# Kernel tuning notes

Measured on AMD Instinct MI355X. Metric: run time of the kernel, lower is better.

## Reference

```python
import jax, jax.numpy as jnp
import numpy as np

B, S, D, H = 8, 2048, 1024, 64

def setup_inputs() -> dict:
    key = jax.random.key(0)
    k1, k2, k3, k4 = jax.random.split(key, 4)
    idx = jax.random.normal(k1, (B, S, D), dtype=jnp.float32)
    # nn.Linear(D, H, bias=False) weights, stored as [D, H] for x @ W
    Wk = jax.random.normal(k2, (D, H), dtype=jnp.float32) * (1.0 / np.sqrt(D))
    Wq = jax.random.normal(k3, (D, H), dtype=jnp.float32) * (1.0 / np.sqrt(D))
    Wv = jax.random.normal(k4, (D, H), dtype=jnp.float32) * (1.0 / np.sqrt(D))
    return {"idx": idx, "Wk": Wk, "Wq": Wq, "Wv": Wv}

def reference(idx, Wk, Wq, Wv):
    b, s, d = idx.shape
    k = idx @ Wk  # [b, s, h]
    q = idx @ Wq
    v = idx @ Wv
    # NOTE: original scales by embedding_dim**-0.5, not head_size**-0.5
    wei = jnp.einsum('bqh,bkh->bqk', q, k) * (d ** -0.5)
    causal = jnp.tril(jnp.ones((s, s), dtype=bool))
    wei = jnp.where(causal, wei, -jnp.inf)
    attn = jax.nn.softmax(wei, axis=-1)  # dropout p=0.0 -> identity
    return jnp.einsum('bqk,bkh->bqh', attn, v)
```

## Files before the change

kernel.cpp:

```cpp
#include <hip/hip_runtime.h>

typedef __attribute__((ext_vector_type(8))) short short8;
typedef __attribute__((ext_vector_type(4))) short short4v;
typedef __attribute__((ext_vector_type(4))) float f32x4;

#define MFMA_16x16x32_BF16(A, B, C) __builtin_amdgcn_mfma_f32_16x16x32_bf16(A, B, C, 0, 0, 0)

__device__ __forceinline__ unsigned short f2bf(float x) {
    unsigned int u = __builtin_bit_cast(unsigned int, x);
    u = (u + 0x7FFFu + ((u >> 16) & 1u)) >> 16;
    return (unsigned short)u;
}

__global__ __launch_bounds__(256) void wconv_kernel(const float* __restrict__ Wk,
                                                    const float* __restrict__ Wq,
                                                    const float* __restrict__ Wv,
                                                    unsigned short* __restrict__ Wt) {
    const int n = blockIdx.x;
    const float* W = (n < 64) ? Wk : (n < 128) ? Wq : Wv;
    const int col = n & 63;
    const int sw = (n & 7) << 3;
    for (int k = threadIdx.x; k < 1024; k += 256) {
        const int kd = (k & ~56) | ((k ^ sw) & 56);
        Wt[(size_t)n * 1024 + kd] = f2bf(W[(size_t)k * 64 + col]);
    }
}

__global__ __launch_bounds__(256) void proj_kernel(const float* __restrict__ X,
                                                   const unsigned short* __restrict__ Wt,
                                                   unsigned short* __restrict__ Kb,
                                                   unsigned short* __restrict__ Qb,
                                                   unsigned short* __restrict__ Vtg) {
    __shared__ __attribute__((aligned(16))) unsigned short Al[32 * 72];
    __shared__ __attribute__((aligned(16))) unsigned short Wl[192 * 64];
    const int t = threadIdx.x;
    const int w = t >> 6, lane = t & 63, lr = lane & 15, g = lane >> 4;
    const int wr = w >> 1, wc = w & 1;
    const int r0 = blockIdx.x * 32;

    f32x4 acc[6] = {};

    const int ar = t >> 3, aj = t & 7;
    const float* xsrc = X + (size_t)(r0 + ar) * 1024 + aj * 8;

    float4 a0 = *(const float4*)xsrc;
    float4 a1 = *(const float4*)(xsrc + 4);
    uint4 aw;
    aw.x = (unsigned)f2bf(a0.x) | ((unsigned)f2bf(a0.y) << 16);
    aw.y = (unsigned)f2bf(a0.z) | ((unsigned)f2bf(a0.w) << 16);
    aw.z = (unsigned)f2bf(a1.x) | ((unsigned)f2bf(a1.y) << 16);
    aw.w = (unsigned)f2bf(a1.z) | ((unsigned)f2bf(a1.w) << 16);

    for (int k0 = 0; k0 < 1024; k0 += 64) {
        __syncthreads();
#pragma unroll
        for (int i = 0; i < 6; ++i) {
            const int q = t + 256 * i;
            const unsigned short* src = Wt + (size_t)(q >> 3) * 1024 + k0 + (q & 7) * 8;
            __builtin_amdgcn_global_load_lds((const __attribute__((address_space(1))) void*)src,
                                             (__attribute__((address_space(3))) void*)&Wl[q * 8],
                                             16, 0, 0);
        }
        *(uint4*)&Al[ar * 72 + aj * 8] = aw;
        __syncthreads();

        const bool more = (k0 + 64) < 1024;
        if (more) {
            a0 = *(const float4*)(xsrc + k0 + 64);
            a1 = *(const float4*)(xsrc + k0 + 68);
        }

        short8 af[2];
        af[0] = *(const short8*)&Al[(16 * wr + lr) * 72 + 8 * g];
        af[1] = *(const short8*)&Al[(16 * wr + lr) * 72 + 32 + 8 * g];
#pragma unroll
        for (int c = 0; c < 6; ++c) {
            const int row = 96 * wc + 16 * c + lr;
#pragma unroll
            for (int sub = 0; sub < 2; ++sub) {
                const int cs = (4 * sub + g) ^ (lr & 7);
                short8 wf = *(const short8*)&Wl[row * 64 + cs * 8];
                acc[c] = MFMA_16x16x32_BF16(af[sub], wf, acc[c]);
            }
        }

        if (more) {
            aw.x = (unsigned)f2bf(a0.x) | ((unsigned)f2bf(a0.y) << 16);
            aw.y = (unsigned)f2bf(a0.z) | ((unsigned)f2bf(a0.w) << 16);
            aw.z = (unsigned)f2bf(a1.x) | ((unsigned)f2bf(a1.y) << 16);
            aw.w = (unsigned)f2bf(a1.z) | ((unsigned)f2bf(a1.w) << 16);
        }
    }

    const int bb = r0 >> 11;
    const int sb0 = (r0 & 2047) + 16 * wr;
    const int row = r0 + 16 * wr + 4 * g;
#pragma unroll
    for (int c = 0; c < 6; ++c) {
        const int n = 96 * wc + 16 * c;
        if (n < 64) {
#pragma unroll
            for (int r = 0; r < 4; ++r)
                Kb[(size_t)(row + r) * 64 + n + lr] = f2bf(acc[c][r]);
        } else if (n < 128) {
#pragma unroll
            for (int r = 0; r < 4; ++r)
                Qb[(size_t)(row + r) * 64 + (n - 64) + lr] = f2bf(acc[c][r]);
        } else {
            const int h = n - 128 + lr;
            uint2 e;
            e.x = (unsigned)f2bf(acc[c][0]) | ((unsigned)f2bf(acc[c][1]) << 16);
            e.y = (unsigned)f2bf(acc[c][2]) | ((unsigned)f2bf(acc[c][3]) << 16);
            *(uint2*)(Vtg + (size_t)bb * 64 * 2048 + (size_t)h * 2048 + sb0 + 4 * g) = e;
        }
    }
}

__global__ __launch_bounds__(512, 2) void attn_kernel(const unsigned short* __restrict__ Kb,
                                                      const unsigned short* __restrict__ Qb,
                                                      const unsigned short* __restrict__ Vtg,
                                                      float* __restrict__ out) {
    __shared__ __attribute__((aligned(16))) float Pacc[16][32][68];
    __shared__ float Pml[2][16][32];

    const int t = threadIdx.x;
    const int w = t >> 6, lane = t & 63;
    const int lr = lane & 15, g = lane >> 4;
    const int p = blockIdx.x, b = blockIdx.y;
    const int nhi = 64 - p;
    const int q0h = (63 - p) * 32, q0l = p * 32;
    const size_t rowbase = (size_t)b * 2048;
    const size_t vbase = (size_t)b * 64 * 2048;
    const float NEG_INF = -__builtin_inff();
    const float SCALE2 = 0.03125f * 1.4426950408889634f;

    short8 qfH[2][2], qfL[2][2];
#pragma unroll
    for (int sub = 0; sub < 2; ++sub)
#pragma unroll
        for (int hh = 0; hh < 2; ++hh) {
            qfH[sub][hh] = *(const short8*)(Qb + (rowbase + q0h + 16 * sub + lr) * 64 + 32 * hh + 8 * g);
            qfL[sub][hh] = *(const short8*)(Qb + (rowbase + q0l + 16 * sub + lr) * 64 + 32 * hh + 8 * g);
        }

    f32x4 accH[2][4] = {}, accL[2][4] = {};
    float mH[2] = {NEG_INF, NEG_INF}, mL[2] = {NEG_INF, NEG_INF};
    float lH[2] = {0.f, 0.f}, lL[2] = {0.f, 0.f};

    const int s0 = (w * 65) >> 3, s1 = ((w + 1) * 65) >> 3;

    auto step = [&](int kv0, int q0, const short8 (&qf)[2][2],
                    f32x4 (&acc)[2][4], float (&m2)[2], float (&ls)[2]) {
        short8 kf[2][2];
#pragma unroll
        for (int f = 0; f < 2; ++f)
#pragma unroll
            for (int hh = 0; hh < 2; ++hh)
                kf[f][hh] = *(const short8*)(Kb + (rowbase + kv0 + 16 * f + lr) * 64 + 32 * hh + 8 * g);
        short8 vf[4];
#pragma unroll
        for (int fh = 0; fh < 4; ++fh) {
            const unsigned short* vp = Vtg + vbase + (size_t)(16 * fh + lr) * 2048 + kv0 + 4 * g;
            short4v v0 = *(const short4v*)vp;
            short4v v1 = *(const short4v*)(vp + 16);
            short8 vv;
            vv[0] = v0[0]; vv[1] = v0[1]; vv[2] = v0[2]; vv[3] = v0[3];
            vv[4] = v1[0]; vv[5] = v1[1]; vv[6] = v1[2]; vv[7] = v1[3];
            vf[fh] = vv;
        }
#pragma unroll
        for (int sub = 0; sub < 2; ++sub) {
            f32x4 sv[2];
#pragma unroll
            for (int f = 0; f < 2; ++f) {
                f32x4 x = {};
                x = MFMA_16x16x32_BF16(kf[f][0], qf[sub][0], x);
                x = MFMA_16x16x32_BF16(kf[f][1], qf[sub][1], x);
                sv[f] = x;
            }
            const int q = q0 + 16 * sub + lr;
            float pvv[8], tmax = NEG_INF;
#pragma unroll
            for (int f = 0; f < 2; ++f)
#pragma unroll
                for (int r = 0; r < 4; ++r) {
                    int kp = kv0 + 16 * f + 4 * g + r;
                    float sc = sv[f][r] * SCALE2;
                    sc = (kp <= q) ? sc : NEG_INF;
                    pvv[4 * f + r] = sc;
                    tmax = fmaxf(tmax, sc);
                }
            tmax = fmaxf(tmax, __shfl_xor(tmax, 16));
            tmax = fmaxf(tmax, __shfl_xor(tmax, 32));
            float mnew = fmaxf(m2[sub], tmax);
            float alpha = exp2f(m2[sub] - mnew);
            float psum = 0.f;
            short8 pf;
#pragma unroll
            for (int e = 0; e < 8; ++e) {
                float pe = exp2f(pvv[e] - mnew);
                psum += pe;
                pf[e] = (short)f2bf(pe);
            }
            psum += __shfl_xor(psum, 16);
            psum += __shfl_xor(psum, 32);
            ls[sub] = ls[sub] * alpha + psum;
            m2[sub] = mnew;
#pragma unroll
            for (int fh = 0; fh < 4; ++fh) {
                acc[sub][fh][0] *= alpha; acc[sub][fh][1] *= alpha;
                acc[sub][fh][2] *= alpha; acc[sub][fh][3] *= alpha;
                acc[sub][fh] = MFMA_16x16x32_BF16(vf[fh], pf, acc[sub][fh]);
            }
        }
    };

    const int ehi = (s1 < nhi) ? s1 : nhi;
    for (int s = s0; s < ehi; ++s) step(s * 32, q0h, qfH, accH, mH, lH);
    const int slo = (s0 > nhi) ? s0 : nhi;
    for (int s = slo; s < s1; ++s) step((s - nhi) * 32, q0l, qfL, accL, mL, lL);

#pragma unroll
    for (int bnd = 0; bnd < 2; ++bnd) {
        const f32x4 (&acc)[2][4] = bnd ? accL : accH;
        const float (&m2)[2] = bnd ? mL : mH;
        const float (&ls)[2] = bnd ? lL : lH;
        const int slot = bnd * 8 + w;
#pragma unroll
        for (int sub = 0; sub < 2; ++sub) {
#pragma unroll
            for (int fh = 0; fh < 4; ++fh)
                *(f32x4*)&Pacc[slot][16 * sub + lr][16 * fh + 4 * g] = acc[sub][fh];
            if (g == 0) {
                Pml[0][slot][16 * sub + lr] = m2[sub];
                Pml[1][slot][16 * sub + lr] = ls[sub];
            }
        }
    }
    __syncthreads();

    {
        const int tb = t >> 8, t2 = t & 255;
        const int qq = t2 & 31, hb = (t2 >> 5) * 8;
        float mw[8], M = NEG_INF;
#pragma unroll
        for (int wv = 0; wv < 8; ++wv) {
            mw[wv] = Pml[0][tb * 8 + wv][qq];
            M = fmaxf(M, mw[wv]);
        }
        float wgt[8], L = 0.f;
#pragma unroll
        for (int wv = 0; wv < 8; ++wv) {
            wgt[wv] = exp2f(mw[wv] - M);
            L += wgt[wv] * Pml[1][tb * 8 + wv][qq];
        }
        f32x4 o0 = {}, o1 = {};
#pragma unroll
        for (int wv = 0; wv < 8; ++wv) {
            f32x4 a0 = *(const f32x4*)&Pacc[tb * 8 + wv][qq][hb];
            f32x4 a1 = *(const f32x4*)&Pacc[tb * 8 + wv][qq][hb + 4];
            o0 += wgt[wv] * a0;
            o1 += wgt[wv] * a1;
        }
        const float invL = 1.f / L;
        o0 *= invL; o1 *= invL;
        const int q0 = tb ? q0l : q0h;
        float* op = out + (rowbase + q0 + qq) * 64 + hb;
        *(f32x4*)op = o0;
        *(f32x4*)(op + 4) = o1;
    }
}

extern "C" void kernel_launch(void* const* d_in, const int* in_sizes, int n_in,
                              void* d_out, int out_size, void* d_ws, size_t ws_size,
                              hipStream_t stream) {
    const float* X  = (const float*)d_in[0];
    const float* Wk = (const float*)d_in[1];
    const float* Wq = (const float*)d_in[2];
    const float* Wv = (const float*)d_in[3];

    unsigned short* Wt  = (unsigned short*)d_ws;
    unsigned short* Kb  = Wt + 192 * 1024;
    unsigned short* Qb  = Kb + 16384 * 64;
    unsigned short* Vtg = Qb + 16384 * 64;
    float* out = (float*)d_out;

    wconv_kernel<<<dim3(192), dim3(256), 0, stream>>>(Wk, Wq, Wv, Wt);
    proj_kernel<<<dim3(512), dim3(256), 0, stream>>>(X, Wt, Kb, Qb, Vtg);
    attn_kernel<<<dim3(32, 8), dim3(512), 0, stream>>>(Kb, Qb, Vtg, out);
}
```

Measured before the change: 58.83 us.

## Split projection columns across blocks and give each attention band its own waves

The projection kernel now launches twice as many blocks, each computing 96 of the 192 output columns. This halves the shared-memory weight tile and the accumulators per block, at the cost of reading each X row tile twice. The attention kernel now uses 1024-thread blocks: eight waves handle the high query band and eight handle the low band, each band splitting its own key range. Previously eight waves shared a combined range of 65 steps, so this doubles per-block parallelism at the cost of larger blocks and possibly lower occupancy per CU.

```diff
diff --git a/kernel.cpp b/kernel.cpp
--- a/kernel.cpp
+++ b/kernel.cpp
@@ -26,19 +26,21 @@
     }
 }
 
-__global__ __launch_bounds__(256) void proj_kernel(const float* __restrict__ X,
-                                                   const unsigned short* __restrict__ Wt,
-                                                   unsigned short* __restrict__ Kb,
-                                                   unsigned short* __restrict__ Qb,
-                                                   unsigned short* __restrict__ Vtg) {
+__global__ __launch_bounds__(256, 4) void proj_kernel(const float* __restrict__ X,
+                                                      const unsigned short* __restrict__ Wt,
+                                                      unsigned short* __restrict__ Kb,
+                                                      unsigned short* __restrict__ Qb,
+                                                      unsigned short* __restrict__ Vtg) {
     __shared__ __attribute__((aligned(16))) unsigned short Al[32 * 72];
-    __shared__ __attribute__((aligned(16))) unsigned short Wl[192 * 64];
+    __shared__ __attribute__((aligned(16))) unsigned short Wl[96 * 64];
     const int t = threadIdx.x;
     const int w = t >> 6, lane = t & 63, lr = lane & 15, g = lane >> 4;
     const int wr = w >> 1, wc = w & 1;
-    const int r0 = blockIdx.x * 32;
-
-    f32x4 acc[6] = {};
+    const int rt = blockIdx.x >> 1, cb = blockIdx.x & 1;
+    const int r0 = rt * 32;
+    const int n0 = cb * 96;
+
+    f32x4 acc[3] = {};
 
     const int ar = t >> 3, aj = t & 7;
     const float* xsrc = X + (size_t)(r0 + ar) * 1024 + aj * 8;
@@ -54,9 +56,9 @@
     for (int k0 = 0; k0 < 1024; k0 += 64) {
         __syncthreads();
 #pragma unroll
-        for (int i = 0; i < 6; ++i) {
+        for (int i = 0; i < 3; ++i) {
             const int q = t + 256 * i;
-            const unsigned short* src = Wt + (size_t)(q >> 3) * 1024 + k0 + (q & 7) * 8;
+            const unsigned short* src = Wt + (size_t)(n0 + (q >> 3)) * 1024 + k0 + (q & 7) * 8;
             __builtin_amdgcn_global_load_lds((const __attribute__((address_space(1))) void*)src,
                                              (__attribute__((address_space(3))) void*)&Wl[q * 8],
                                              16, 0, 0);
@@ -74,8 +76,8 @@
         af[0] = *(const short8*)&Al[(16 * wr + lr) * 72 + 8 * g];
         af[1] = *(const short8*)&Al[(16 * wr + lr) * 72 + 32 + 8 * g];
 #pragma unroll
-        for (int c = 0; c < 6; ++c) {
-            const int row = 96 * wc + 16 * c + lr;
+        for (int c = 0; c < 3; ++c) {
+            const int row = 48 * wc + 16 * c + lr;
 #pragma unroll
             for (int sub = 0; sub < 2; ++sub) {
                 const int cs = (4 * sub + g) ^ (lr & 7);
@@ -93,33 +95,33 @@
     }
 
     const int bb = r0 >> 11;
-    const int sb0 = (r0 & 2047) + 16 * wr;
+    const int sb0 = (r0 & 2047) + 16 * wr + 4 * g;
     const int row = r0 + 16 * wr + 4 * g;
 #pragma unroll
-    for (int c = 0; c < 6; ++c) {
-        const int n = 96 * wc + 16 * c;
-        if (n < 64) {
+    for (int i = 0; i < 3; ++i) {
+        const int cg = cb * 6 + wc * 3 + i;
+        if (cg < 4) {
 #pragma unroll
             for (int r = 0; r < 4; ++r)
-                Kb[(size_t)(row + r) * 64 + n + lr] = f2bf(acc[c][r]);
-        } else if (n < 128) {
+                Kb[(size_t)(row + r) * 64 + 16 * cg + lr] = f2bf(acc[i][r]);
+        } else if (cg < 8) {
 #pragma unroll
             for (int r = 0; r < 4; ++r)
-                Qb[(size_t)(row + r) * 64 + (n - 64) + lr] = f2bf(acc[c][r]);
+                Qb[(size_t)(row + r) * 64 + 16 * (cg - 4) + lr] = f2bf(acc[i][r]);
         } else {
-            const int h = n - 128 + lr;
+            const int h = 16 * (cg - 8) + lr;
             uint2 e;
-            e.x = (unsigned)f2bf(acc[c][0]) | ((unsigned)f2bf(acc[c][1]) << 16);
-            e.y = (unsigned)f2bf(acc[c][2]) | ((unsigned)f2bf(acc[c][3]) << 16);
-            *(uint2*)(Vtg + (size_t)bb * 64 * 2048 + (size_t)h * 2048 + sb0 + 4 * g) = e;
-        }
-    }
-}
-
-__global__ __launch_bounds__(512, 2) void attn_kernel(const unsigned short* __restrict__ Kb,
-                                                      const unsigned short* __restrict__ Qb,
-                                                      const unsigned short* __restrict__ Vtg,
-                                                      float* __restrict__ out) {
+            e.x = (unsigned)f2bf(acc[i][0]) | ((unsigned)f2bf(acc[i][1]) << 16);
+            e.y = (unsigned)f2bf(acc[i][2]) | ((unsigned)f2bf(acc[i][3]) << 16);
+            *(uint2*)(Vtg + (size_t)bb * 64 * 2048 + (size_t)h * 2048 + sb0) = e;
+        }
+    }
+}
+
+__global__ __launch_bounds__(1024, 4) void attn_kernel(const unsigned short* __restrict__ Kb,
+                                                       const unsigned short* __restrict__ Qb,
+                                                       const unsigned short* __restrict__ Vtg,
+                                                       float* __restrict__ out) {
     __shared__ __attribute__((aligned(16))) float Pacc[16][32][68];
     __shared__ float Pml[2][16][32];
 
@@ -127,30 +129,29 @@
     const int w = t >> 6, lane = t & 63;
     const int lr = lane & 15, g = lane >> 4;
     const int p = blockIdx.x, b = blockIdx.y;
-    const int nhi = 64 - p;
-    const int q0h = (63 - p) * 32, q0l = p * 32;
+    const int band = w >> 3, wi = w & 7;
+    const int nb = band ? (p + 1) : (64 - p);
+    const int q0 = band ? p * 32 : (63 - p) * 32;
     const size_t rowbase = (size_t)b * 2048;
     const size_t vbase = (size_t)b * 64 * 2048;
     const float NEG_INF = -__builtin_inff();
     const float SCALE2 = 0.03125f * 1.4426950408889634f;
 
-    short8 qfH[2][2], qfL[2][2];
+    short8 qf[2][2];
 #pragma unroll
     for (int sub = 0; sub < 2; ++sub)
 #pragma unroll
-        for (int hh = 0; hh < 2; ++hh) {
-            qfH[sub][hh] = *(const short8*)(Qb + (rowbase + q0h + 16 * sub + lr) * 64 + 32 * hh + 8 * g);
-            qfL[sub][hh] = *(const short8*)(Qb + (rowbase + q0l + 16 * sub + lr) * 64 + 32 * hh + 8 * g);
-        }
-
-    f32x4 accH[2][4] = {}, accL[2][4] = {};
-    float mH[2] = {NEG_INF, NEG_INF}, mL[2] = {NEG_INF, NEG_INF};
-    float lH[2] = {0.f, 0.f}, lL[2] = {0.f, 0.f};
-
-    const int s0 = (w * 65) >> 3, s1 = ((w + 1) * 65) >> 3;
-
-    auto step = [&](int kv0, int q0, const short8 (&qf)[2][2],
-                    f32x4 (&acc)[2][4], float (&m2)[2], float (&ls)[2]) {
+        for (int hh = 0; hh < 2; ++hh)
+            qf[sub][hh] = *(const short8*)(Qb + (rowbase + q0 + 16 * sub + lr) * 64 + 32 * hh + 8 * g);
+
+    f32x4 acc[2][4] = {};
+    float m2[2] = {NEG_INF, NEG_INF};
+    float ls[2] = {0.f, 0.f};
+
+    const int s0 = (wi * nb) >> 3, s1 = ((wi + 1) * nb) >> 3;
+
+    for (int s = s0; s < s1; ++s) {
+        const int kv0 = s * 32;
         short8 kf[2][2];
 #pragma unroll
         for (int f = 0; f < 2; ++f)
@@ -213,19 +214,10 @@
                 acc[sub][fh] = MFMA_16x16x32_BF16(vf[fh], pf, acc[sub][fh]);
             }
         }
-    };
-
-    const int ehi = (s1 < nhi) ? s1 : nhi;
-    for (int s = s0; s < ehi; ++s) step(s * 32, q0h, qfH, accH, mH, lH);
-    const int slo = (s0 > nhi) ? s0 : nhi;
-    for (int s = slo; s < s1; ++s) step((s - nhi) * 32, q0l, qfL, accL, mL, lL);
-
-#pragma unroll
-    for (int bnd = 0; bnd < 2; ++bnd) {
-        const f32x4 (&acc)[2][4] = bnd ? accL : accH;
-        const float (&m2)[2] = bnd ? mL : mH;
-        const float (&ls)[2] = bnd ? lL : lH;
-        const int slot = bnd * 8 + w;
+    }
+
+    {
+        const int slot = band * 8 + wi;
 #pragma unroll
         for (int sub = 0; sub < 2; ++sub) {
 #pragma unroll
@@ -240,8 +232,8 @@
     __syncthreads();
 
     {
-        const int tb = t >> 8, t2 = t & 255;
-        const int qq = t2 & 31, hb = (t2 >> 5) * 8;
+        const int tb = t >> 9, t2 = t & 511;
+        const int qq = t2 & 31, hb = (t2 >> 5) * 4;
         float mw[8], M = NEG_INF;
 #pragma unroll
         for (int wv = 0; wv < 8; ++wv) {
@@ -254,20 +246,13 @@
             wgt[wv] = exp2f(mw[wv] - M);
             L += wgt[wv] * Pml[1][tb * 8 + wv][qq];
         }
-        f32x4 o0 = {}, o1 = {};
-#pragma unroll
-        for (int wv = 0; wv < 8; ++wv) {
-            f32x4 a0 = *(const f32x4*)&Pacc[tb * 8 + wv][qq][hb];
-            f32x4 a1 = *(const f32x4*)&Pacc[tb * 8 + wv][qq][hb + 4];
-            o0 += wgt[wv] * a0;
-            o1 += wgt[wv] * a1;
-        }
-        const float invL = 1.f / L;
-        o0 *= invL; o1 *= invL;
-        const int q0 = tb ? q0l : q0h;
-        float* op = out + (rowbase + q0 + qq) * 64 + hb;
-        *(f32x4*)op = o0;
-        *(f32x4*)(op + 4) = o1;
+        f32x4 o = {};
+#pragma unroll
+        for (int wv = 0; wv < 8; ++wv)
+            o += wgt[wv] * *(const f32x4*)&Pacc[tb * 8 + wv][qq][hb];
+        o *= (1.f / L);
+        const int qb = tb ? p * 32 : (63 - p) * 32;
+        *(f32x4*)(out + (rowbase + qb + qq) * 64 + hb) = o;
     }
 }
 
@@ -286,6 +271,6 @@
     float* out = (float*)d_out;
 
     wconv_kernel<<<dim3(192), dim3(256), 0, stream>>>(Wk, Wq, Wv, Wt);
-    proj_kernel<<<dim3(512), dim3(256), 0, stream>>>(X, Wt, Kb, Qb, Vtg);
-    attn_kernel<<<dim3(32, 8), dim3(512), 0, stream>>>(Kb, Qb, Vtg, out);
-}
+    proj_kernel<<<dim3(1024), dim3(256), 0, stream>>>(X, Wt, Kb, Qb, Vtg);
+    attn_kernel<<<dim3(32, 8), dim3(1024), 0, stream>>>(Kb, Qb, Vtg, out);
+}
```

Result: slower. 61.68 us (+4.8%).

## Split projection columns across two blocks and stream X into LDS asynchronously

Applied to the files above, without the earlier changes.

The projection kernel now launches twice as many blocks, each computing 96 of the 192 output columns for a 32-row tile. Each block reads X through asynchronous global-to-LDS loads of fp32 data with an XOR swizzle and converts it to bf16 when reading fragments, replacing the old register prefetch and convert path. This raises parallelism and shrinks per-block LDS and accumulator use, but every X tile is now read from global memory twice (once per column half), and the loads are no longer overlapped with the previous iteration's compute.

```diff
diff --git a/kernel.cpp b/kernel.cpp
--- a/kernel.cpp
+++ b/kernel.cpp
@@ -31,51 +31,58 @@
                                                    unsigned short* __restrict__ Kb,
                                                    unsigned short* __restrict__ Qb,
                                                    unsigned short* __restrict__ Vtg) {
-    __shared__ __attribute__((aligned(16))) unsigned short Al[32 * 72];
-    __shared__ __attribute__((aligned(16))) unsigned short Wl[192 * 64];
+    __shared__ __attribute__((aligned(16))) float Af[32 * 64];
+    __shared__ __attribute__((aligned(16))) unsigned short Wl[96 * 64];
     const int t = threadIdx.x;
     const int w = t >> 6, lane = t & 63, lr = lane & 15, g = lane >> 4;
     const int wr = w >> 1, wc = w & 1;
-    const int r0 = blockIdx.x * 32;
-
-    f32x4 acc[6] = {};
-
-    const int ar = t >> 3, aj = t & 7;
-    const float* xsrc = X + (size_t)(r0 + ar) * 1024 + aj * 8;
-
-    float4 a0 = *(const float4*)xsrc;
-    float4 a1 = *(const float4*)(xsrc + 4);
-    uint4 aw;
-    aw.x = (unsigned)f2bf(a0.x) | ((unsigned)f2bf(a0.y) << 16);
-    aw.y = (unsigned)f2bf(a0.z) | ((unsigned)f2bf(a0.w) << 16);
-    aw.z = (unsigned)f2bf(a1.x) | ((unsigned)f2bf(a1.y) << 16);
-    aw.w = (unsigned)f2bf(a1.z) | ((unsigned)f2bf(a1.w) << 16);
-
-    for (int k0 = 0; k0 < 1024; k0 += 64) {
+    const int rt = blockIdx.x >> 1, cb = blockIdx.x & 1;
+    const int r0 = rt * 32;
+    const int n0 = cb * 96;
+
+    f32x4 acc[3] = {};
+
+    for (int t16 = 0; t16 < 16; ++t16) {
+        const int k0 = t16 * 64;
         __syncthreads();
 #pragma unroll
-        for (int i = 0; i < 6; ++i) {
+        for (int i = 0; i < 2; ++i) {
             const int q = t + 256 * i;
-            const unsigned short* src = Wt + (size_t)(q >> 3) * 1024 + k0 + (q & 7) * 8;
+            const int r = q >> 4, c = q & 15;
+            const int csrc = c ^ ((r & 7) << 1);
+            const float* src = X + (size_t)(r0 + r) * 1024 + k0 + csrc * 4;
+            __builtin_amdgcn_global_load_lds((const __attribute__((address_space(1))) void*)src,
+                                             (__attribute__((address_space(3))) void*)&Af[q * 4],
+                                             16, 0, 0);
+        }
+#pragma unroll
+        for (int i = 0; i < 3; ++i) {
+            const int q = t + 256 * i;
+            const unsigned short* src = Wt + (size_t)(n0 + (q >> 3)) * 1024 + k0 + (q & 7) * 8;
             __builtin_amdgcn_global_load_lds((const __attribute__((address_space(1))) void*)src,
                                              (__attribute__((address_space(3))) void*)&Wl[q * 8],
                                              16, 0, 0);
         }
-        *(uint4*)&Al[ar * 72 + aj * 8] = aw;
         __syncthreads();
 
-        const bool more = (k0 + 64) < 1024;
-        if (more) {
-            a0 = *(const float4*)(xsrc + k0 + 64);
-            a1 = *(const float4*)(xsrc + k0 + 68);
-        }
-
+        const int ar = 16 * wr + lr;
         short8 af[2];
-        af[0] = *(const short8*)&Al[(16 * wr + lr) * 72 + 8 * g];
-        af[1] = *(const short8*)&Al[(16 * wr + lr) * 72 + 32 + 8 * g];
-#pragma unroll
-        for (int c = 0; c < 6; ++c) {
-            const int row = 96 * wc + 16 * c + lr;
+#pragma unroll
+        for (int sub = 0; sub < 2; ++sub) {
+            const int cs0 = (8 * sub + 2 * g) ^ ((lr & 7) << 1);
+            const float* ap = &Af[ar * 64 + cs0 * 4];
+            float4 v0 = *(const float4*)ap;
+            float4 v1 = *(const float4*)(ap + 4);
+            short8 a;
+            a[0] = (short)f2bf(v0.x); a[1] = (short)f2bf(v0.y);
+            a[2] = (short)f2bf(v0.z); a[3] = (short)f2bf(v0.w);
+            a[4] = (short)f2bf(v1.x); a[5] = (short)f2bf(v1.y);
+            a[6] = (short)f2bf(v1.z); a[7] = (short)f2bf(v1.w);
+            af[sub] = a;
+        }
+#pragma unroll
+        for (int c = 0; c < 3; ++c) {
+            const int row = 48 * wc + 16 * c + lr;
 #pragma unroll
             for (int sub = 0; sub < 2; ++sub) {
                 const int cs = (4 * sub + g) ^ (lr & 7);
@@ -83,35 +90,28 @@
                 acc[c] = MFMA_16x16x32_BF16(af[sub], wf, acc[c]);
             }
         }
-
-        if (more) {
-            aw.x = (unsigned)f2bf(a0.x) | ((unsigned)f2bf(a0.y) << 16);
-            aw.y = (unsigned)f2bf(a0.z) | ((unsigned)f2bf(a0.w) << 16);
-            aw.z = (unsigned)f2bf(a1.x) | ((unsigned)f2bf(a1.y) << 16);
-            aw.w = (unsigned)f2bf(a1.z) | ((unsigned)f2bf(a1.w) << 16);
-        }
     }
 
     const int bb = r0 >> 11;
-    const int sb0 = (r0 & 2047) + 16 * wr;
+    const int sb0 = (r0 & 2047) + 16 * wr + 4 * g;
     const int row = r0 + 16 * wr + 4 * g;
 #pragma unroll
-    for (int c = 0; c < 6; ++c) {
-        const int n = 96 * wc + 16 * c;
-        if (n < 64) {
+    for (int i = 0; i < 3; ++i) {
+        const int cg = cb * 6 + wc * 3 + i;
+        if (cg < 4) {
 #pragma unroll
             for (int r = 0; r < 4; ++r)
-                Kb[(size_t)(row + r) * 64 + n + lr] = f2bf(acc[c][r]);
-        } else if (n < 128) {
+                Kb[(size_t)(row + r) * 64 + 16 * cg + lr] = f2bf(acc[i][r]);
+        } else if (cg < 8) {
 #pragma unroll
             for (int r = 0; r < 4; ++r)
-                Qb[(size_t)(row + r) * 64 + (n - 64) + lr] = f2bf(acc[c][r]);
+                Qb[(size_t)(row + r) * 64 + 16 * (cg - 4) + lr] = f2bf(acc[i][r]);
         } else {
-            const int h = n - 128 + lr;
+            const int h = 16 * (cg - 8) + lr;
             uint2 e;
-            e.x = (unsigned)f2bf(acc[c][0]) | ((unsigned)f2bf(acc[c][1]) << 16);
-            e.y = (unsigned)f2bf(acc[c][2]) | ((unsigned)f2bf(acc[c][3]) << 16);
-            *(uint2*)(Vtg + (size_t)bb * 64 * 2048 + (size_t)h * 2048 + sb0 + 4 * g) = e;
+            e.x = (unsigned)f2bf(acc[i][0]) | ((unsigned)f2bf(acc[i][1]) << 16);
+            e.y = (unsigned)f2bf(acc[i][2]) | ((unsigned)f2bf(acc[i][3]) << 16);
+            *(uint2*)(Vtg + (size_t)bb * 64 * 2048 + (size_t)h * 2048 + sb0) = e;
         }
     }
 }
@@ -286,6 +286,6 @@
     float* out = (float*)d_out;
 
     wconv_kernel<<<dim3(192), dim3(256), 0, stream>>>(Wk, Wq, Wv, Wt);
-    proj_kernel<<<dim3(512), dim3(256), 0, stream>>>(X, Wt, Kb, Qb, Vtg);
+    proj_kernel<<<dim3(1024), dim3(256), 0, stream>>>(X, Wt, Kb, Qb, Vtg);
     attn_kernel<<<dim3(32, 8), dim3(512), 0, stream>>>(Kb, Qb, Vtg, out);
 }
```

New measurement: 61.93 us. 1.05x slower.
